# Kernel tuning notes

Hardware: AMD Instinct MI355X
Metric: run time of the kernel (lower is better)

The kernel has to match this reference:

```python
import jax, jax.numpy as jnp
import numpy as np

WINDOW_SIZES = (4, 8)
NUM_HEADS = 8


def _rel_pos_index(ws):
    # Swin-style relative position index, (ws*ws, ws*ws) int array (constant).
    coords = np.stack(np.meshgrid(np.arange(ws), np.arange(ws), indexing='ij')).reshape(2, -1)
    rel = (coords[:, :, None] - coords[:, None, :]).transpose(1, 2, 0)
    rel[..., 0] += ws - 1
    rel[..., 1] += ws - 1
    rel[..., 0] *= 2 * ws - 1
    return jnp.asarray(rel.sum(-1))


def setup_inputs() -> dict:
    key = jax.random.key(0)
    ks = jax.random.split(key, 4)
    b, l, hx, wy, w1, w2, d = 4, 4, 8, 8, 8, 8, 256
    gh = NUM_HEADS // len(WINDOW_SIZES)
    x = jax.random.normal(ks[0], (b, l, hx, wy, w1, w2, d), jnp.float32)
    qkv_w = jax.random.normal(ks[1], (3 * d, d), jnp.float32) * 0.02  # torch Linear weight (out,in)
    qkv_b = jnp.zeros((3 * d,), jnp.float32)
    bias_table_0 = jax.random.normal(ks[2], ((2 * WINDOW_SIZES[0] - 1) ** 2, gh), jnp.float32) * 0.02
    bias_table_1 = jax.random.normal(ks[3], ((2 * WINDOW_SIZES[1] - 1) ** 2, gh), jnp.float32) * 0.02
    return {"x": x, "qkv_w": qkv_w, "qkv_b": qkv_b,
            "bias_table_0": bias_table_0, "bias_table_1": bias_table_1}


def _forward(x, qkv_w, qkv_b, tables):
    b, l, hx, wy, w1, w2, d = x.shape
    H, W = hx * w1, wy * w2
    ng = len(WINDOW_SIZES)
    channel = d // ng
    gh = NUM_HEADS // ng
    gc = channel // gh
    # rearrange 'b l x y w1 w2 d -> (b x y) (l w1 w2) d'
    xf = jnp.transpose(x, (0, 2, 3, 1, 4, 5, 6)).reshape(b * hx * wy, l * w1 * w2, d)
    B, HW, C = xf.shape
    qkv = xf @ qkv_w.T + qkv_b                               # (B, HW, 3C)
    qkv = jnp.transpose(qkv.reshape(B, HW, 3, C), (2, 0, 1, 3))
    # faithful raw reshape as in the torch code (layout remap, not semantic rearrange)
    qkv = qkv.reshape(3, l * b, H, W, C)
    outs = []
    for i, ws in enumerate(WINDOW_SIZES):
        g = qkv[..., i * channel:(i + 1) * channel]          # (3, Bg, H, W, channel)
        pad_r = (ws - W % ws) % ws
        pad_b = (ws - H % ws) % ws
        g = jnp.pad(g, ((0, 0), (0, 0), (0, pad_b), (0, pad_r), (0, 0)))
        Bg = l * b
        Hp, Wp = H + pad_b, W + pad_r
        N = ws * ws
        # window partition -> (3, B_, gh, N, gc)
        gw = g.reshape(3, Bg, Hp // ws, ws, Wp // ws, ws, channel)
        gw = jnp.transpose(gw, (0, 1, 2, 4, 3, 5, 6)).reshape(3, -1, N, gh, gc)
        gw = jnp.transpose(gw, (0, 1, 3, 2, 4))
        q, k, v = gw[0], gw[1], gw[2]
        attn = jnp.einsum('bhnd,bhmd->bhnm', q * (gc ** -0.5), k)
        idx = _rel_pos_index(ws)
        bias = tables[i][idx.reshape(-1)].reshape(N, N, gh)
        bias = jnp.transpose(bias, (2, 0, 1))                # (gh, N, N)
        attn = jax.nn.softmax(attn + bias[None], axis=-1)
        o = jnp.einsum('bhnm,bhmd->bnhd', attn, v).reshape(-1, N, channel)
        # window reverse
        o = o.reshape(Bg, Hp // ws, Wp // ws, ws, ws, channel)
        o = jnp.transpose(o, (0, 1, 3, 2, 4, 5)).reshape(Bg, Hp, Wp, channel)[:, :H, :W, :]
        outs.append(o)
    out = jnp.concatenate(outs, -1)                          # (Bg, H, W, d)
    out = jnp.transpose(out.reshape(B, d, HW), (0, 2, 1))    # faithful raw reshape
    # rearrange '(b x y) (l w1 w2) d -> b l x y w1 w2 d'
    return jnp.transpose(out.reshape(b, hx, wy, l, w1, w2, d), (0, 3, 1, 2, 4, 5, 6))


def reference(x, qkv_w, qkv_b, bias_table_0, bias_table_1):
    return _forward(x, qkv_w, qkv_b, (bias_table_0, bias_table_1))
```

## Files before the change

kernel.cpp:

```cpp
#include <hip/hip_runtime.h>

typedef unsigned short u16;
typedef unsigned int u32;
typedef __attribute__((ext_vector_type(8))) short short8;
typedef __attribute__((ext_vector_type(4))) float f32x4;
typedef __attribute__((ext_vector_type(4))) float fvec4;
typedef __attribute__((ext_vector_type(4))) u16 u16x4;

typedef __attribute__((address_space(1))) void gvoid;
typedef __attribute__((address_space(3))) void lvoid;

__device__ __forceinline__ u16 f2bf(float f) {
  u32 u = __float_as_uint(f);
  u += 0x7FFFu + ((u >> 16) & 1u);
  return (u16)(u >> 16);
}

__device__ __forceinline__ void gl16(const u16* g, u16* d) {
  __builtin_amdgcn_global_load_lds((gvoid*)g, (lvoid*)d, 16, 0, 0);
}

__device__ __forceinline__ void wave_lds_fence() {
  asm volatile("s_waitcnt lgkmcnt(0)" ::: "memory");
  __builtin_amdgcn_sched_barrier(0);
}

__device__ __forceinline__ int m_of(int Bg, int h, int w) {
  return ((Bg >> 2) << 14) | ((h & 3) << 12) | ((((Bg & 3) << 1) | (h >> 5)) << 9) |
         (((h >> 2) & 7) << 6) | w;
}

__device__ __forceinline__ f32x4 mfma16(short8 a, short8 b, f32x4 c) {
  return __builtin_amdgcn_mfma_f32_16x16x32_bf16(a, b, c, 0, 0, 0);
}

__device__ __forceinline__ short8 ld8(const u16* __restrict__ qb, int c4, int m) {
  union { u16x4 h[2]; short8 v; } u;
  u.h[0] = *(const u16x4*)(qb + (size_t)c4 * 262144 + (size_t)m * 4);
  u.h[1] = *(const u16x4*)(qb + (size_t)(c4 + 1) * 262144 + (size_t)m * 4);
  return u.v;
}

__global__ void k_prep(const float* __restrict__ qkv_w, const float* __restrict__ t0,
                       const float* __restrict__ t1, u16* __restrict__ wbp,
                       float* __restrict__ bias4, float* __restrict__ bias8) {
  int tid = blockIdx.x * 256 + threadIdx.x;
  int stride = gridDim.x * 256;
  for (int i = tid; i < 196608; i += stride) {
    int nhc = i / 12288;
    int rem = i - nhc * 12288;
    int p = rem >> 3, e = rem & 7;
    int cu = p >> 2;
    int su = (p & 3) ^ ((cu >> 1) & 3);
    int col = (nhc >> 3) * 384 + cu;
    int k = (nhc & 7) * 32 + su * 8 + e;
    wbp[i] = f2bf(qkv_w[col * 256 + k]);
  }
  for (int i = tid; i < 4 * 64 * 64; i += stride) {
    int g = i >> 12, n = (i >> 6) & 63, m = i & 63;
    int di = (n >> 3) - (m >> 3) + 7, dj = (n & 7) - (m & 7) + 7;
    bias8[i] = t1[(di * 15 + dj) * 4 + g];
  }
  for (int i = tid; i < 4 * 16 * 16; i += stride) {
    int g = i >> 8, n = (i >> 4) & 15, m = i & 15;
    int di = (n >> 2) - (m >> 2) + 3, dj = (n & 3) - (m & 3) + 3;
    bias4[i] = t0[(di * 7 + dj) * 4 + g];
  }
}

__global__ __launch_bounds__(512, 4) void k_gemm(const float* __restrict__ x,
                                                 const u16* __restrict__ wbp,
                                                 const float* __restrict__ qkv_b,
                                                 u16* __restrict__ qkvB) {
  __shared__ __align__(16) u16 As[64 * 128];
  __shared__ __align__(16) u16 Bs[2 * 8 * 1536];
  const int t = threadIdx.x;
  const int wid = t >> 6, l = t & 63;
  const int lr = l & 15, lk4 = l >> 4;
  const int mt = ((blockIdx.x >> 4) << 3) | (blockIdx.x & 7);
  const int nh = (blockIdx.x >> 3) & 1;
  const size_t xbase = (size_t)mt * 64 * 256;
  const int colbase = nh * 384;

  const u16* wsrc = wbp + (size_t)(nh * 8) * 12288 + (wid * 192 + l) * 8;
  u16* bdst = &Bs[wid * 1536];

  const int sr0 = t >> 5;
  const int scc = (t & 31) * 4;
  const int sslot = scc >> 3, shalf = scc & 7;

  fvec4 bb[3];
#pragma unroll
  for (int jt = 0; jt < 3; ++jt)
    bb[jt] = *(const fvec4*)(qkv_b + colbase + wid * 48 + jt * 16 + lk4 * 4);
  asm volatile("" ::: "memory");

#pragma unroll
  for (int j = 0; j < 3; ++j) gl16(wsrc + j * 512, bdst + j * 512);
#pragma unroll
  for (int j = 0; j < 3; ++j) gl16(wsrc + 12288 + j * 512, bdst + 12288 + j * 512);
  asm volatile("" ::: "memory");

  {
    const float* xp = x + xbase + (size_t)sr0 * 256 + scc;
#pragma unroll
    for (int j = 0; j < 4; ++j) {
      fvec4 v = *(const fvec4*)(xp + j * 16 * 256);
      int r = sr0 + j * 16;
      u16x4 u;
      u[0] = f2bf(v[0]); u[1] = f2bf(v[1]); u[2] = f2bf(v[2]); u[3] = f2bf(v[3]);
      *(u16x4*)&As[r * 128 + ((sslot ^ (r & 7)) << 3) + shalf] = u;
    }
  }
  asm volatile("s_waitcnt lgkmcnt(0)" ::: "memory");
  __builtin_amdgcn_s_barrier();

  f32x4 acc[3][4];
  const f32x4 z = {0.f, 0.f, 0.f, 0.f};
#pragma unroll
  for (int jt = 0; jt < 3; ++jt)
#pragma unroll
    for (int rt = 0; rt < 4; ++rt) acc[jt][rt] = z;

  const int bswz = (lr >> 1) & 3;
#pragma unroll
  for (int ci = 0; ci < 8; ++ci) {
    if (ci == 4) {
      __builtin_amdgcn_s_barrier();
      __builtin_amdgcn_sched_barrier(0);
      {
        const float* xp1 = x + xbase + (size_t)sr0 * 256 + 128 + scc;
#pragma unroll
        for (int j = 0; j < 4; ++j) {
          fvec4 v = *(const fvec4*)(xp1 + j * 16 * 256);
          int r = sr0 + j * 16;
          u16x4 u;
          u[0] = f2bf(v[0]); u[1] = f2bf(v[1]); u[2] = f2bf(v[2]); u[3] = f2bf(v[3]);
          *(u16x4*)&As[r * 128 + ((sslot ^ (r & 7)) << 3) + shalf] = u;
        }
      }
      asm volatile("s_waitcnt lgkmcnt(0)" ::: "memory");
      __builtin_amdgcn_sched_barrier(0);
      __builtin_amdgcn_s_barrier();
    }
    const int buf = ci & 1;
    if (ci == 7) asm volatile("s_waitcnt vmcnt(0)" ::: "memory");
    else         asm volatile("s_waitcnt vmcnt(3)" ::: "memory");
    __builtin_amdgcn_sched_barrier(0);
    short8 a[4], b[3];
    const int kslot = (ci & 3) * 4 + lk4;
#pragma unroll
    for (int rt = 0; rt < 4; ++rt) {
      int row = rt * 16 + lr;
      a[rt] = *(const short8*)&As[row * 128 + ((kslot ^ (row & 7)) << 3)];
    }
#pragma unroll
    for (int jt = 0; jt < 3; ++jt)
      b[jt] = *(const short8*)&Bs[buf * 12288 + wid * 1536 +
                                  (jt * 16 + lr) * 32 + ((lk4 ^ bswz) * 8)];
    asm volatile("s_waitcnt lgkmcnt(0)" ::: "memory");
    __builtin_amdgcn_sched_barrier(0);
    if (ci < 6) {
      const u16* s = wsrc + (size_t)(ci + 2) * 12288;
      u16* d = bdst + buf * 12288;
#pragma unroll
      for (int j = 0; j < 3; ++j) gl16(s + j * 512, d + j * 512);
    }
    __builtin_amdgcn_sched_barrier(0);
#pragma unroll
    for (int jt = 0; jt < 3; ++jt)
#pragma unroll
      for (int rt = 0; rt < 4; ++rt)
        acc[jt][rt] = mfma16(b[jt], a[rt], acc[jt][rt]);
  }

  const int rows0 = mt * 64;
#pragma unroll
  for (int jt = 0; jt < 3; ++jt) {
    int col0 = colbase + wid * 48 + jt * 16 + lk4 * 4;
    int c40 = col0 >> 2;
#pragma unroll
    for (int rt = 0; rt < 4; ++rt) {
      int row = rows0 + rt * 16 + lr;
      u16x4 u;
#pragma unroll
      for (int r = 0; r < 4; ++r) u[r] = f2bf(acc[jt][rt][r] + bb[jt][r]);
      *(u16x4*)&qkvB[(size_t)c40 * 262144 + (size_t)row * 4] = u;
    }
  }
}

__global__ __launch_bounds__(64) void k_attn8(const u16* __restrict__ qkvB,
                                              const float* __restrict__ bias8,
                                              float* __restrict__ out) {
  __shared__ __align__(16) u16 vtg[32 * 72];
  __shared__ __align__(16) u16 plg[64 * 72];
  const int lid = blockIdx.x;
  const int logical = (lid & 7) * 512 + (lid >> 3);
  const int g = logical & 3;
  const int wj = (logical >> 2) & 7, wi = (logical >> 5) & 7, Bg = logical >> 8;
  const int h0 = wi * 8, w0 = wj * 8;
  const int l = threadIdx.x;
  const int lr = l & 15, lk4 = l >> 4;

  const int c4q = 32 + g * 8 + lk4 * 2;
  const int c4k = 96 + g * 8 + lk4 * 2;
  short8 aq[4], bk[4];
#pragma unroll
  for (int tn = 0; tn < 4; ++tn) {
    int n = tn * 16 + lr;
    int m = m_of(Bg, h0 + (n >> 3), w0 + (n & 7));
    aq[tn] = ld8(qkvB, c4q, m);
    bk[tn] = ld8(qkvB, c4k, m);
  }
  {
    int m = m_of(Bg, h0 + (l >> 3), w0 + (l & 7));
#pragma unroll
    for (int j2 = 0; j2 < 8; ++j2) {
      u16x4 p = *(const u16x4*)(qkvB + (size_t)(160 + g * 8 + j2) * 262144 + (size_t)m * 4);
#pragma unroll
      for (int r = 0; r < 4; ++r) vtg[(j2 * 4 + r) * 72 + l] = p[r];
    }
  }
  f32x4 z = {0.f, 0.f, 0.f, 0.f};
  f32x4 s[4][4];
#pragma unroll
  for (int tn = 0; tn < 4; ++tn)
#pragma unroll
    for (int tm = 0; tm < 4; ++tm) s[tn][tm] = mfma16(aq[tn], bk[tm], z);

  const float scale = 0.17677669529663687f;
#pragma unroll
  for (int tn = 0; tn < 4; ++tn)
#pragma unroll
    for (int tm = 0; tm < 4; ++tm)
#pragma unroll
      for (int r = 0; r < 4; ++r) {
        int n = tn * 16 + lk4 * 4 + r, m = tm * 16 + lr;
        s[tn][tm][r] = s[tn][tm][r] * scale + bias8[(g * 64 + n) * 64 + m];
      }
  float invden[4][4];
#pragma unroll
  for (int tn = 0; tn < 4; ++tn)
#pragma unroll
    for (int r = 0; r < 4; ++r) {
      float mx = fmaxf(fmaxf(s[tn][0][r], s[tn][1][r]), fmaxf(s[tn][2][r], s[tn][3][r]));
#pragma unroll
      for (int d = 1; d < 16; d <<= 1) mx = fmaxf(mx, __shfl_xor(mx, d));
      float sum = 0.f;
#pragma unroll
      for (int tm = 0; tm < 4; ++tm) {
        float p = __expf(s[tn][tm][r] - mx);
        s[tn][tm][r] = p;
        sum += p;
      }
#pragma unroll
      for (int d = 1; d < 16; d <<= 1) sum += __shfl_xor(sum, d);
      invden[tn][r] = 1.f / sum;
    }
#pragma unroll
  for (int tn = 0; tn < 4; ++tn)
#pragma unroll
    for (int tm = 0; tm < 4; ++tm)
#pragma unroll
      for (int r = 0; r < 4; ++r)
        plg[(tn * 16 + lk4 * 4 + r) * 72 + tm * 16 + lr] = f2bf(s[tn][tm][r]);
  wave_lds_fence();
  f32x4 o[4][2];
#pragma unroll
  for (int tn = 0; tn < 4; ++tn) { o[tn][0] = z; o[tn][1] = z; }
#pragma unroll
  for (int kc = 0; kc < 2; ++kc) {
    short8 pa[4], vb[2];
#pragma unroll
    for (int tn = 0; tn < 4; ++tn)
      pa[tn] = *(const short8*)&plg[(tn * 16 + lr) * 72 + kc * 32 + lk4 * 8];
#pragma unroll
    for (int te = 0; te < 2; ++te)
      vb[te] = *(const short8*)&vtg[(te * 16 + lr) * 72 + kc * 32 + lk4 * 8];
#pragma unroll
    for (int tn = 0; tn < 4; ++tn)
#pragma unroll
      for (int te = 0; te < 2; ++te) o[tn][te] = mfma16(pa[tn], vb[te], o[tn][te]);
  }
  wave_lds_fence();
  float* ol = (float*)plg;
#pragma unroll
  for (int tn = 0; tn < 4; ++tn)
#pragma unroll
    for (int te = 0; te < 2; ++te)
#pragma unroll
      for (int r = 0; r < 4; ++r) {
        int n = tn * 16 + lk4 * 4 + r;
        ol[n * 33 + te * 16 + lr] = o[tn][te][r] * invden[tn][r];
      }
  wave_lds_fence();
  {
    int h = h0 + (l >> 3), w = w0 + (l & 7);
    size_t base = ((size_t)(Bg >> 2)) * 4194304 + (size_t)(((Bg & 3) * 2 + (h >> 5))) * 131072 +
                  (size_t)(((h >> 2) & 7)) * 16384 + (size_t)((h & 3) * 64 + w);
#pragma unroll
    for (int e = 0; e < 32; ++e) {
      int c = 128 + g * 32 + e;
      size_t idx = base + (size_t)(c >> 6) * 1048576 + (size_t)((c >> 3) & 7) * 2048 +
                   (size_t)(c & 7) * 256;
      out[idx] = ol[l * 33 + e];
    }
  }
}

__global__ __launch_bounds__(64) void k_attn4(const u16* __restrict__ qkvB,
                                              const float* __restrict__ bias4,
                                              float* __restrict__ out) {
  __shared__ __align__(16) u16 vtw[32 * 40];
  __shared__ __align__(16) u16 plw[16 * 40];
  __shared__ __align__(16) float olw[16 * 33];
  const int lid = blockIdx.x;
  const int logical = (lid & 7) * 2048 + (lid >> 3);
  const int g = logical & 3;
  const int wid2 = logical >> 2;
  const int Bg = wid2 >> 8, wi = (wid2 >> 4) & 15, wj = wid2 & 15;
  const int h0 = wi * 4, w0 = wj * 4;
  const int l = threadIdx.x;
  const int lr = l & 15, lk4 = l >> 4;
  const f32x4 z = {0.f, 0.f, 0.f, 0.f};
  const short8 z8 = {0, 0, 0, 0, 0, 0, 0, 0};
  const float scale = 0.17677669529663687f;

  {
    u16x4 z4 = {0, 0, 0, 0};
    *(u16x4*)&plw[(l & 15) * 40 + 16 + (l >> 4) * 4] = z4;
    *(short8*)&vtw[(l >> 1) * 40 + 16 + (l & 1) * 8] = z8;
  }
  const int mq = m_of(Bg, h0 + (lr >> 2), w0 + (lr & 3));

  short8 aq = ld8(qkvB, g * 8 + lk4 * 2, mq);
  short8 bk = ld8(qkvB, 64 + g * 8 + lk4 * 2, mq);
  {
    short8 v = ld8(qkvB, 128 + g * 8 + lk4 * 2, mq);
#pragma unroll
    for (int j = 0; j < 8; ++j) vtw[(lk4 * 8 + j) * 40 + lr] = (u16)v[j];
  }
  f32x4 s = mfma16(aq, bk, z);
#pragma unroll
  for (int r = 0; r < 4; ++r) {
    int n = lk4 * 4 + r;
    s[r] = s[r] * scale + bias4[(g * 16 + n) * 16 + lr];
  }
  float invden[4];
#pragma unroll
  for (int r = 0; r < 4; ++r) {
    float mx = s[r];
#pragma unroll
    for (int d = 1; d < 16; d <<= 1) mx = fmaxf(mx, __shfl_xor(mx, d));
    float p = __expf(s[r] - mx);
    s[r] = p;
    float sum = p;
#pragma unroll
    for (int d = 1; d < 16; d <<= 1) sum += __shfl_xor(sum, d);
    invden[r] = 1.f / sum;
  }
#pragma unroll
  for (int r = 0; r < 4; ++r) plw[(lk4 * 4 + r) * 40 + lr] = f2bf(s[r]);
  wave_lds_fence();
  f32x4 o[2];
#pragma unroll
  for (int te = 0; te < 2; ++te) {
    short8 pa = *(const short8*)&plw[lr * 40 + lk4 * 8];
    short8 vb = *(const short8*)&vtw[(te * 16 + lr) * 40 + lk4 * 8];
    o[te] = mfma16(pa, vb, z);
  }
#pragma unroll
  for (int te = 0; te < 2; ++te)
#pragma unroll
    for (int r = 0; r < 4; ++r) {
      int n = lk4 * 4 + r;
      olw[n * 33 + te * 16 + lr] = o[te][r] * invden[r];
    }
  wave_lds_fence();
  {
    int h = h0 + (lr >> 2), w = w0 + (lr & 3);
    size_t base = ((size_t)(Bg >> 2)) * 4194304 +
                  (size_t)(((Bg & 3) * 2 + (h >> 5))) * 131072 +
                  (size_t)(((h >> 2) & 7)) * 16384 + (size_t)((h & 3) * 64 + w);
#pragma unroll
    for (int ee = 0; ee < 8; ++ee) {
      int e = lk4 * 8 + ee;
      int c = g * 32 + e;
      size_t idx = base + (size_t)(c >> 6) * 1048576 + (size_t)((c >> 3) & 7) * 2048 +
                   (size_t)(c & 7) * 256;
      out[idx] = olw[lr * 33 + e];
    }
  }
}

extern "C" void kernel_launch(void* const* d_in, const int* in_sizes, int n_in,
                              void* d_out, int out_size, void* d_ws, size_t ws_size,
                              hipStream_t stream) {
  const float* x = (const float*)d_in[0];
  const float* qkv_w = (const float*)d_in[1];
  const float* qkv_b = (const float*)d_in[2];
  const float* t0 = (const float*)d_in[3];
  const float* t1 = (const float*)d_in[4];
  float* out = (float*)d_out;
  char* ws = (char*)d_ws;

  u16* qkvB = (u16*)ws;
  u16* wbp = (u16*)(ws + 100663296);
  float* bias8 = (float*)(ws + 101056512);
  float* bias4 = (float*)(ws + 101122048);

  k_prep<<<256, 256, 0, stream>>>(qkv_w, t0, t1, wbp, bias4, bias8);
  k_gemm<<<2048, 512, 0, stream>>>(x, wbp, qkv_b, qkvB);
  k_attn8<<<4096, 64, 0, stream>>>(qkvB, bias8, out);
  k_attn4<<<16384, 64, 0, stream>>>(qkvB, bias4, out);
}
```

Measured before the change: 95.28 us.

## Merge attention kernels into one launch and load full A tile upfront in GEMM

The two windowed-attention kernels (8x8 and 4x4 windows) are merged into a single launch that branches on block index, so one kernel launch and its tail are removed and both window sizes can run concurrently. The GEMM now stages the whole 64x256 bf16 activation tile in LDS before the K loop instead of loading it in two halves with an extra barrier pair mid-loop. This doubles the A-tile LDS footprint, which may reduce GEMM occupancy. The merged attention kernel sizes its shared buffer for the larger branch.

```diff
diff --git a/kernel.cpp b/kernel.cpp
--- a/kernel.cpp
+++ b/kernel.cpp
@@ -72,7 +72,7 @@
                                                  const u16* __restrict__ wbp,
                                                  const float* __restrict__ qkv_b,
                                                  u16* __restrict__ qkvB) {
-  __shared__ __align__(16) u16 As[64 * 128];
+  __shared__ __align__(16) u16 As[64 * 256];
   __shared__ __align__(16) u16 Bs[2 * 8 * 1536];
   const int t = threadIdx.x;
   const int wid = t >> 6, l = t & 63;
@@ -85,10 +85,6 @@
   const u16* wsrc = wbp + (size_t)(nh * 8) * 12288 + (wid * 192 + l) * 8;
   u16* bdst = &Bs[wid * 1536];
 
-  const int sr0 = t >> 5;
-  const int scc = (t & 31) * 4;
-  const int sslot = scc >> 3, shalf = scc & 7;
-
   fvec4 bb[3];
 #pragma unroll
   for (int jt = 0; jt < 3; ++jt)
@@ -102,14 +98,16 @@
   asm volatile("" ::: "memory");
 
   {
-    const float* xp = x + xbase + (size_t)sr0 * 256 + scc;
-#pragma unroll
-    for (int j = 0; j < 4; ++j) {
-      fvec4 v = *(const fvec4*)(xp + j * 16 * 256);
-      int r = sr0 + j * 16;
+    const int cc = (l & 63) * 4;
+    const int slot = cc >> 3, half = cc & 7;
+    const float* xp = x + xbase + (size_t)wid * 256 + cc;
+#pragma unroll
+    for (int it = 0; it < 8; ++it) {
+      fvec4 v = *(const fvec4*)(xp + it * 8 * 256);
+      int r = wid + it * 8;
       u16x4 u;
       u[0] = f2bf(v[0]); u[1] = f2bf(v[1]); u[2] = f2bf(v[2]); u[3] = f2bf(v[3]);
-      *(u16x4*)&As[r * 128 + ((sslot ^ (r & 7)) << 3) + shalf] = u;
+      *(u16x4*)&As[r * 256 + ((slot ^ (r & 7)) << 3) + half] = u;
     }
   }
   asm volatile("s_waitcnt lgkmcnt(0)" ::: "memory");
@@ -125,34 +123,16 @@
   const int bswz = (lr >> 1) & 3;
 #pragma unroll
   for (int ci = 0; ci < 8; ++ci) {
-    if (ci == 4) {
-      __builtin_amdgcn_s_barrier();
-      __builtin_amdgcn_sched_barrier(0);
-      {
-        const float* xp1 = x + xbase + (size_t)sr0 * 256 + 128 + scc;
-#pragma unroll
-        for (int j = 0; j < 4; ++j) {
-          fvec4 v = *(const fvec4*)(xp1 + j * 16 * 256);
-          int r = sr0 + j * 16;
-          u16x4 u;
-          u[0] = f2bf(v[0]); u[1] = f2bf(v[1]); u[2] = f2bf(v[2]); u[3] = f2bf(v[3]);
-          *(u16x4*)&As[r * 128 + ((sslot ^ (r & 7)) << 3) + shalf] = u;
-        }
-      }
-      asm volatile("s_waitcnt lgkmcnt(0)" ::: "memory");
-      __builtin_amdgcn_sched_barrier(0);
-      __builtin_amdgcn_s_barrier();
-    }
     const int buf = ci & 1;
     if (ci == 7) asm volatile("s_waitcnt vmcnt(0)" ::: "memory");
     else         asm volatile("s_waitcnt vmcnt(3)" ::: "memory");
     __builtin_amdgcn_sched_barrier(0);
     short8 a[4], b[3];
-    const int kslot = (ci & 3) * 4 + lk4;
+    const int kslot = ci * 4 + lk4;
 #pragma unroll
     for (int rt = 0; rt < 4; ++rt) {
       int row = rt * 16 + lr;
-      a[rt] = *(const short8*)&As[row * 128 + ((kslot ^ (row & 7)) << 3)];
+      a[rt] = *(const short8*)&As[row * 256 + ((kslot ^ (row & 7)) << 3)];
     }
 #pragma unroll
     for (int jt = 0; jt < 3; ++jt)
@@ -190,206 +170,203 @@
   }
 }
 
-__global__ __launch_bounds__(64) void k_attn8(const u16* __restrict__ qkvB,
-                                              const float* __restrict__ bias8,
-                                              float* __restrict__ out) {
-  __shared__ __align__(16) u16 vtg[32 * 72];
-  __shared__ __align__(16) u16 plg[64 * 72];
-  const int lid = blockIdx.x;
-  const int logical = (lid & 7) * 512 + (lid >> 3);
-  const int g = logical & 3;
-  const int wj = (logical >> 2) & 7, wi = (logical >> 5) & 7, Bg = logical >> 8;
-  const int h0 = wi * 8, w0 = wj * 8;
-  const int l = threadIdx.x;
-  const int lr = l & 15, lk4 = l >> 4;
-
-  const int c4q = 32 + g * 8 + lk4 * 2;
-  const int c4k = 96 + g * 8 + lk4 * 2;
-  short8 aq[4], bk[4];
-#pragma unroll
-  for (int tn = 0; tn < 4; ++tn) {
-    int n = tn * 16 + lr;
-    int m = m_of(Bg, h0 + (n >> 3), w0 + (n & 7));
-    aq[tn] = ld8(qkvB, c4q, m);
-    bk[tn] = ld8(qkvB, c4k, m);
-  }
-  {
-    int m = m_of(Bg, h0 + (l >> 3), w0 + (l & 7));
-#pragma unroll
-    for (int j2 = 0; j2 < 8; ++j2) {
-      u16x4 p = *(const u16x4*)(qkvB + (size_t)(160 + g * 8 + j2) * 262144 + (size_t)m * 4);
-#pragma unroll
-      for (int r = 0; r < 4; ++r) vtg[(j2 * 4 + r) * 72 + l] = p[r];
-    }
-  }
-  f32x4 z = {0.f, 0.f, 0.f, 0.f};
-  f32x4 s[4][4];
-#pragma unroll
-  for (int tn = 0; tn < 4; ++tn)
-#pragma unroll
-    for (int tm = 0; tm < 4; ++tm) s[tn][tm] = mfma16(aq[tn], bk[tm], z);
-
-  const float scale = 0.17677669529663687f;
-#pragma unroll
-  for (int tn = 0; tn < 4; ++tn)
-#pragma unroll
-    for (int tm = 0; tm < 4; ++tm)
-#pragma unroll
-      for (int r = 0; r < 4; ++r) {
-        int n = tn * 16 + lk4 * 4 + r, m = tm * 16 + lr;
-        s[tn][tm][r] = s[tn][tm][r] * scale + bias8[(g * 64 + n) * 64 + m];
-      }
-  float invden[4][4];
-#pragma unroll
-  for (int tn = 0; tn < 4; ++tn)
-#pragma unroll
-    for (int r = 0; r < 4; ++r) {
-      float mx = fmaxf(fmaxf(s[tn][0][r], s[tn][1][r]), fmaxf(s[tn][2][r], s[tn][3][r]));
-#pragma unroll
-      for (int d = 1; d < 16; d <<= 1) mx = fmaxf(mx, __shfl_xor(mx, d));
-      float sum = 0.f;
-#pragma unroll
-      for (int tm = 0; tm < 4; ++tm) {
-        float p = __expf(s[tn][tm][r] - mx);
-        s[tn][tm][r] = p;
-        sum += p;
-      }
-#pragma unroll
-      for (int d = 1; d < 16; d <<= 1) sum += __shfl_xor(sum, d);
-      invden[tn][r] = 1.f / sum;
-    }
-#pragma unroll
-  for (int tn = 0; tn < 4; ++tn)
-#pragma unroll
-    for (int tm = 0; tm < 4; ++tm)
-#pragma unroll
-      for (int r = 0; r < 4; ++r)
-        plg[(tn * 16 + lk4 * 4 + r) * 72 + tm * 16 + lr] = f2bf(s[tn][tm][r]);
-  wave_lds_fence();
-  f32x4 o[4][2];
-#pragma unroll
-  for (int tn = 0; tn < 4; ++tn) { o[tn][0] = z; o[tn][1] = z; }
-#pragma unroll
-  for (int kc = 0; kc < 2; ++kc) {
-    short8 pa[4], vb[2];
-#pragma unroll
-    for (int tn = 0; tn < 4; ++tn)
-      pa[tn] = *(const short8*)&plg[(tn * 16 + lr) * 72 + kc * 32 + lk4 * 8];
-#pragma unroll
-    for (int te = 0; te < 2; ++te)
-      vb[te] = *(const short8*)&vtg[(te * 16 + lr) * 72 + kc * 32 + lk4 * 8];
-#pragma unroll
-    for (int tn = 0; tn < 4; ++tn)
-#pragma unroll
-      for (int te = 0; te < 2; ++te) o[tn][te] = mfma16(pa[tn], vb[te], o[tn][te]);
-  }
-  wave_lds_fence();
-  float* ol = (float*)plg;
-#pragma unroll
-  for (int tn = 0; tn < 4; ++tn)
-#pragma unroll
-    for (int te = 0; te < 2; ++te)
-#pragma unroll
-      for (int r = 0; r < 4; ++r) {
-        int n = tn * 16 + lk4 * 4 + r;
-        ol[n * 33 + te * 16 + lr] = o[tn][te][r] * invden[tn][r];
-      }
-  wave_lds_fence();
-  {
-    int h = h0 + (l >> 3), w = w0 + (l & 7);
-    size_t base = ((size_t)(Bg >> 2)) * 4194304 + (size_t)(((Bg & 3) * 2 + (h >> 5))) * 131072 +
-                  (size_t)(((h >> 2) & 7)) * 16384 + (size_t)((h & 3) * 64 + w);
-#pragma unroll
-    for (int e = 0; e < 32; ++e) {
-      int c = 128 + g * 32 + e;
-      size_t idx = base + (size_t)(c >> 6) * 1048576 + (size_t)((c >> 3) & 7) * 2048 +
-                   (size_t)(c & 7) * 256;
-      out[idx] = ol[l * 33 + e];
-    }
-  }
-}
-
-__global__ __launch_bounds__(64) void k_attn4(const u16* __restrict__ qkvB,
-                                              const float* __restrict__ bias4,
-                                              float* __restrict__ out) {
-  __shared__ __align__(16) u16 vtw[32 * 40];
-  __shared__ __align__(16) u16 plw[16 * 40];
-  __shared__ __align__(16) float olw[16 * 33];
-  const int lid = blockIdx.x;
-  const int logical = (lid & 7) * 2048 + (lid >> 3);
-  const int g = logical & 3;
-  const int wid2 = logical >> 2;
-  const int Bg = wid2 >> 8, wi = (wid2 >> 4) & 15, wj = wid2 & 15;
-  const int h0 = wi * 4, w0 = wj * 4;
+__global__ __launch_bounds__(64) void k_attn(const u16* __restrict__ qkvB,
+                                             const float* __restrict__ bias8,
+                                             const float* __restrict__ bias4,
+                                             float* __restrict__ out) {
+  __shared__ __align__(16) u16 sbuf[6912];
   const int l = threadIdx.x;
   const int lr = l & 15, lk4 = l >> 4;
   const f32x4 z = {0.f, 0.f, 0.f, 0.f};
-  const short8 z8 = {0, 0, 0, 0, 0, 0, 0, 0};
   const float scale = 0.17677669529663687f;
 
-  {
-    u16x4 z4 = {0, 0, 0, 0};
-    *(u16x4*)&plw[(l & 15) * 40 + 16 + (l >> 4) * 4] = z4;
-    *(short8*)&vtw[(l >> 1) * 40 + 16 + (l & 1) * 8] = z8;
-  }
-  const int mq = m_of(Bg, h0 + (lr >> 2), w0 + (lr & 3));
-
-  short8 aq = ld8(qkvB, g * 8 + lk4 * 2, mq);
-  short8 bk = ld8(qkvB, 64 + g * 8 + lk4 * 2, mq);
-  {
-    short8 v = ld8(qkvB, 128 + g * 8 + lk4 * 2, mq);
-#pragma unroll
-    for (int j = 0; j < 8; ++j) vtw[(lk4 * 8 + j) * 40 + lr] = (u16)v[j];
-  }
-  f32x4 s = mfma16(aq, bk, z);
-#pragma unroll
-  for (int r = 0; r < 4; ++r) {
-    int n = lk4 * 4 + r;
-    s[r] = s[r] * scale + bias4[(g * 16 + n) * 16 + lr];
-  }
-  float invden[4];
-#pragma unroll
-  for (int r = 0; r < 4; ++r) {
-    float mx = s[r];
-#pragma unroll
-    for (int d = 1; d < 16; d <<= 1) mx = fmaxf(mx, __shfl_xor(mx, d));
-    float p = __expf(s[r] - mx);
-    s[r] = p;
-    float sum = p;
-#pragma unroll
-    for (int d = 1; d < 16; d <<= 1) sum += __shfl_xor(sum, d);
-    invden[r] = 1.f / sum;
-  }
-#pragma unroll
-  for (int r = 0; r < 4; ++r) plw[(lk4 * 4 + r) * 40 + lr] = f2bf(s[r]);
-  wave_lds_fence();
-  f32x4 o[2];
-#pragma unroll
-  for (int te = 0; te < 2; ++te) {
-    short8 pa = *(const short8*)&plw[lr * 40 + lk4 * 8];
-    short8 vb = *(const short8*)&vtw[(te * 16 + lr) * 40 + lk4 * 8];
-    o[te] = mfma16(pa, vb, z);
-  }
-#pragma unroll
-  for (int te = 0; te < 2; ++te)
+  if (blockIdx.x < 4096) {
+    u16* vtg = sbuf;
+    u16* plg = sbuf + 2304;
+    const int lid = blockIdx.x;
+    const int logical = (lid & 7) * 512 + (lid >> 3);
+    const int g = logical & 3;
+    const int wj = (logical >> 2) & 7, wi = (logical >> 5) & 7, Bg = logical >> 8;
+    const int h0 = wi * 8, w0 = wj * 8;
+
+    const int c4q = 32 + g * 8 + lk4 * 2;
+    const int c4k = 96 + g * 8 + lk4 * 2;
+    short8 aq[4], bk[4];
+#pragma unroll
+    for (int tn = 0; tn < 4; ++tn) {
+      int n = tn * 16 + lr;
+      int m = m_of(Bg, h0 + (n >> 3), w0 + (n & 7));
+      aq[tn] = ld8(qkvB, c4q, m);
+      bk[tn] = ld8(qkvB, c4k, m);
+    }
+    {
+      int m = m_of(Bg, h0 + (l >> 3), w0 + (l & 7));
+#pragma unroll
+      for (int j2 = 0; j2 < 8; ++j2) {
+        u16x4 p = *(const u16x4*)(qkvB + (size_t)(160 + g * 8 + j2) * 262144 + (size_t)m * 4);
+#pragma unroll
+        for (int r = 0; r < 4; ++r) vtg[(j2 * 4 + r) * 72 + l] = p[r];
+      }
+    }
+    f32x4 s[4][4];
+#pragma unroll
+    for (int tn = 0; tn < 4; ++tn)
+#pragma unroll
+      for (int tm = 0; tm < 4; ++tm) s[tn][tm] = mfma16(aq[tn], bk[tm], z);
+
+#pragma unroll
+    for (int tn = 0; tn < 4; ++tn)
+#pragma unroll
+      for (int tm = 0; tm < 4; ++tm)
+#pragma unroll
+        for (int r = 0; r < 4; ++r) {
+          int n = tn * 16 + lk4 * 4 + r, m = tm * 16 + lr;
+          s[tn][tm][r] = s[tn][tm][r] * scale + bias8[(g * 64 + n) * 64 + m];
+        }
+    float invden[4][4];
+#pragma unroll
+    for (int tn = 0; tn < 4; ++tn)
+#pragma unroll
+      for (int r = 0; r < 4; ++r) {
+        float mx = fmaxf(fmaxf(s[tn][0][r], s[tn][1][r]), fmaxf(s[tn][2][r], s[tn][3][r]));
+#pragma unroll
+        for (int d = 1; d < 16; d <<= 1) mx = fmaxf(mx, __shfl_xor(mx, d));
+        float sum = 0.f;
+#pragma unroll
+        for (int tm = 0; tm < 4; ++tm) {
+          float p = __expf(s[tn][tm][r] - mx);
+          s[tn][tm][r] = p;
+          sum += p;
+        }
+#pragma unroll
+        for (int d = 1; d < 16; d <<= 1) sum += __shfl_xor(sum, d);
+        invden[tn][r] = 1.f / sum;
+      }
+#pragma unroll
+    for (int tn = 0; tn < 4; ++tn)
+#pragma unroll
+      for (int tm = 0; tm < 4; ++tm)
+#pragma unroll
+        for (int r = 0; r < 4; ++r)
+          plg[(tn * 16 + lk4 * 4 + r) * 72 + tm * 16 + lr] = f2bf(s[tn][tm][r]);
+    wave_lds_fence();
+    f32x4 o[4][2];
+#pragma unroll
+    for (int tn = 0; tn < 4; ++tn) { o[tn][0] = z; o[tn][1] = z; }
+#pragma unroll
+    for (int kc = 0; kc < 2; ++kc) {
+      short8 pa[4], vb[2];
+#pragma unroll
+      for (int tn = 0; tn < 4; ++tn)
+        pa[tn] = *(const short8*)&plg[(tn * 16 + lr) * 72 + kc * 32 + lk4 * 8];
+#pragma unroll
+      for (int te = 0; te < 2; ++te)
+        vb[te] = *(const short8*)&vtg[(te * 16 + lr) * 72 + kc * 32 + lk4 * 8];
+#pragma unroll
+      for (int tn = 0; tn < 4; ++tn)
+#pragma unroll
+        for (int te = 0; te < 2; ++te) o[tn][te] = mfma16(pa[tn], vb[te], o[tn][te]);
+    }
+    wave_lds_fence();
+    float* ol = (float*)plg;
+#pragma unroll
+    for (int tn = 0; tn < 4; ++tn)
+#pragma unroll
+      for (int te = 0; te < 2; ++te)
+#pragma unroll
+        for (int r = 0; r < 4; ++r) {
+          int n = tn * 16 + lk4 * 4 + r;
+          ol[n * 33 + te * 16 + lr] = o[tn][te][r] * invden[tn][r];
+        }
+    wave_lds_fence();
+    {
+      int h = h0 + (l >> 3), w = w0 + (l & 7);
+      size_t base = ((size_t)(Bg >> 2)) * 4194304 + (size_t)(((Bg & 3) * 2 + (h >> 5))) * 131072 +
+                    (size_t)(((h >> 2) & 7)) * 16384 + (size_t)((h & 3) * 64 + w);
+#pragma unroll
+      for (int e = 0; e < 32; ++e) {
+        int c = 128 + g * 32 + e;
+        size_t idx = base + (size_t)(c >> 6) * 1048576 + (size_t)((c >> 3) & 7) * 2048 +
+                     (size_t)(c & 7) * 256;
+        out[idx] = ol[l * 33 + e];
+      }
+    }
+  } else {
+    u16* vtw = sbuf;
+    u16* plw = sbuf + 1280;
+    float* olw = (float*)(sbuf + 1920);
+    const int lid = blockIdx.x - 4096;
+    const int logical = (lid & 7) * 2048 + (lid >> 3);
+    const int g = logical & 3;
+    const int wid2 = logical >> 2;
+    const int Bg = wid2 >> 8, wi = (wid2 >> 4) & 15, wj = wid2 & 15;
+    const int h0 = wi * 4, w0 = wj * 4;
+    const short8 z8 = {0, 0, 0, 0, 0, 0, 0, 0};
+
+    {
+      u16x4 z4 = {0, 0, 0, 0};
+      *(u16x4*)&plw[(l & 15) * 40 + 16 + (l >> 4) * 4] = z4;
+      *(short8*)&vtw[(l >> 1) * 40 + 16 + (l & 1) * 8] = z8;
+    }
+    const int mq = m_of(Bg, h0 + (lr >> 2), w0 + (lr & 3));
+
+    short8 aq = ld8(qkvB, g * 8 + lk4 * 2, mq);
+    short8 bk = ld8(qkvB, 64 + g * 8 + lk4 * 2, mq);
+    {
+      short8 v = ld8(qkvB, 128 + g * 8 + lk4 * 2, mq);
+#pragma unroll
+      for (int j = 0; j < 8; ++j) vtw[(lk4 * 8 + j) * 40 + lr] = (u16)v[j];
+    }
+    f32x4 s = mfma16(aq, bk, z);
 #pragma unroll
     for (int r = 0; r < 4; ++r) {
       int n = lk4 * 4 + r;
-      olw[n * 33 + te * 16 + lr] = o[te][r] * invden[r];
-    }
-  wave_lds_fence();
-  {
-    int h = h0 + (lr >> 2), w = w0 + (lr & 3);
-    size_t base = ((size_t)(Bg >> 2)) * 4194304 +
-                  (size_t)(((Bg & 3) * 2 + (h >> 5))) * 131072 +
-                  (size_t)(((h >> 2) & 7)) * 16384 + (size_t)((h & 3) * 64 + w);
-#pragma unroll
-    for (int ee = 0; ee < 8; ++ee) {
-      int e = lk4 * 8 + ee;
-      int c = g * 32 + e;
-      size_t idx = base + (size_t)(c >> 6) * 1048576 + (size_t)((c >> 3) & 7) * 2048 +
-                   (size_t)(c & 7) * 256;
-      out[idx] = olw[lr * 33 + e];
+      s[r] = s[r] * scale + bias4[(g * 16 + n) * 16 + lr];
+    }
+    float invden[4];
+#pragma unroll
+    for (int r = 0; r < 4; ++r) {
+      float mx = s[r];
+#pragma unroll
+      for (int d = 1; d < 16; d <<= 1) mx = fmaxf(mx, __shfl_xor(mx, d));
+      float p = __expf(s[r] - mx);
+      s[r] = p;
+      float sum = p;
+#pragma unroll
+      for (int d = 1; d < 16; d <<= 1) sum += __shfl_xor(sum, d);
+      invden[r] = 1.f / sum;
+    }
+#pragma unroll
+    for (int r = 0; r < 4; ++r) plw[(lk4 * 4 + r) * 40 + lr] = f2bf(s[r]);
+    wave_lds_fence();
+    f32x4 o[2];
+#pragma unroll
+    for (int te = 0; te < 2; ++te) {
+      short8 pa = *(const short8*)&plw[lr * 40 + lk4 * 8];
+      short8 vb = *(const short8*)&vtw[(te * 16 + lr) * 40 + lk4 * 8];
+      o[te] = mfma16(pa, vb, z);
+    }
+#pragma unroll
+    for (int te = 0; te < 2; ++te)
+#pragma unroll
+      for (int r = 0; r < 4; ++r) {
+        int n = lk4 * 4 + r;
+        olw[n * 33 + te * 16 + lr] = o[te][r] * invden[r];
+      }
+    wave_lds_fence();
+    {
+      int h = h0 + (lr >> 2), w = w0 + (lr & 3);
+      size_t base = ((size_t)(Bg >> 2)) * 4194304 +
+                    (size_t)(((Bg & 3) * 2 + (h >> 5))) * 131072 +
+                    (size_t)(((h >> 2) & 7)) * 16384 + (size_t)((h & 3) * 64 + w);
+#pragma unroll
+      for (int ee = 0; ee < 8; ++ee) {
+        int e = lk4 * 8 + ee;
+        int c = g * 32 + e;
+        size_t idx = base + (size_t)(c >> 6) * 1048576 + (size_t)((c >> 3) & 7) * 2048 +
+                     (size_t)(c & 7) * 256;
+        out[idx] = olw[lr * 33 + e];
+      }
     }
   }
 }
@@ -412,6 +389,5 @@
 
   k_prep<<<256, 256, 0, stream>>>(qkv_w, t0, t1, wbp, bias4, bias8);
   k_gemm<<<2048, 512, 0, stream>>>(x, wbp, qkv_b, qkvB);
-  k_attn8<<<4096, 64, 0, stream>>>(qkvB, bias8, out);
-  k_attn4<<<16384, 64, 0, stream>>>(qkvB, bias4, out);
-}
+  k_attn<<<20480, 64, 0, stream>>>(qkvB, bias8, bias4, out);
+}
```

After: 93.77 us. About the same (-1.6%).
